# Performance work log

Measured on AMD Instinct MI355X. Metric: run time of the kernel, lower is better.

The kernel has to match this reference:

```python
import jax, jax.numpy as jnp
import numpy as np

MARGIN = 0.2
PAIR_EPS = 1e-6   # torch pairwise_distance eps inside TripletMarginLoss
NORM_EPS = 1e-12  # F.normalize eps


def setup_inputs() -> dict:
    key = jax.random.key(0)
    k1, k2, k3 = jax.random.split(key, 3)
    bs, C, D = 64, 1024, 64
    inputs = jax.random.normal(k1, (bs, C, D), dtype=jnp.float32)
    label = jax.random.randint(k2, (bs, C, 1), 0, 2).astype(jnp.float32)
    prot = jax.random.normal(k3, (C, D), dtype=jnp.float32)
    prot = prot / jnp.linalg.norm(prot, axis=1, keepdims=True)
    return {"inputs": inputs, "label": label, "pos_prot": prot, "only_update": 0}


def reference(inputs, label, pos_prot, only_update):
    bs, C, D = inputs.shape
    # F.normalize(p=2, dim=1) per class slice == normalize over last dim of [bs,C,D]
    nrm = jnp.linalg.norm(inputs, axis=-1, keepdims=True)
    x = inputs / jnp.maximum(nrm, NORM_EPS)                      # [bs,C,D]

    # torch.cdist(x, prot): euclidean distances [bs, C(anchor cls), C(prot)]
    x2 = jnp.sum(x * x, axis=-1)                                 # [bs,C]
    p2 = jnp.sum(pos_prot * pos_prot, axis=-1)                   # [C]
    xp = jnp.einsum('bcd,kd->bck', x, pos_prot)                  # [bs,C,C]
    d2 = x2[:, :, None] + p2[None, None, :] - 2.0 * xp
    prot_dist = jnp.sqrt(jnp.maximum(d2, 0.0))                   # [bs,C,C]

    # hard negative: nearest prototype excluding the anchor's own class
    # (argsort + skip-self loop == masked argmin)
    eye = jnp.eye(C, dtype=bool)[None, :, :]
    neg_cls = jnp.argmin(jnp.where(eye, jnp.inf, prot_dist), axis=-1)  # [bs,C]

    positives = pos_prot[None, :, :]                             # [1,C,D] (broadcast of repeat)
    negatives = pos_prot[neg_cls]                                # [bs,C,D]

    # TripletMarginLoss(margin=0.2, p=2, reduction='none'), eps inside distance
    d_ap = jnp.linalg.norm(x - positives + PAIR_EPS, axis=-1)    # [bs,C]
    d_an = jnp.linalg.norm(x - negatives + PAIR_EPS, axis=-1)    # [bs,C]
    tri = jnp.maximum(d_ap - d_an + MARGIN, 0.0)                 # [bs,C]

    w = label[:, :, 0]                                           # [bs,C]
    loss = jnp.mean(jnp.sum(tri * w, axis=-1) / jnp.sum(w, axis=-1))
    return loss
```

## Files before the change

kernel.cpp:

```cpp
#include <hip/hip_runtime.h>
#include <cfloat>

#define BS 64
#define C  1024
#define D  64
#define CT 128

typedef __attribute__((ext_vector_type(8))) short short8;
typedef __attribute__((ext_vector_type(4))) float f32x4;
typedef unsigned short ushort_t;
typedef unsigned int uint_t;

__device__ __forceinline__ ushort_t f2bf(float f) {
    uint_t u = __float_as_uint(f);
    u += 0x7fffu + ((u >> 16) & 1u);
    return (ushort_t)(u >> 16);
}

__global__ void prep_prot(const float* __restrict__ prot, ushort_t* __restrict__ ph)
{
    const int k = blockIdx.x * 128 + threadIdx.x;
    const float4* row = (const float4*)(prot + (size_t)k * D);
    const int jt = k >> 4;
    #pragma unroll
    for (int dg = 0; dg < 8; dg++) {
        float4 a = row[dg * 2];
        float4 b = row[dg * 2 + 1];
        float x[8] = {a.x, a.y, a.z, a.w, b.x, b.y, b.z, b.w};
        short8 hv;
        #pragma unroll
        for (int e = 0; e < 8; e++) hv[e] = (short)f2bf(x[e]);
        const int h  = dg >> 2;
        const int ln = (k & 15) + (dg & 3) * 16;
        ((short8*)ph)[(size_t)jt * 128 + h * 64 + ln] = hv;
    }
}

__global__ __launch_bounds__(512, 4)
void triplet_mfma(const float* __restrict__ inputs,
                  const float* __restrict__ label,
                  const float* __restrict__ prot,
                  const ushort_t* __restrict__ phg,
                  float* __restrict__ part)
{
    __shared__ short8 xh[1024];
    __shared__ float  invn[CT];
    __shared__ uint_t redk[CT][4];
    __shared__ float  snum[512], sden[512];

    const int tid  = threadIdx.x;
    const int lane = tid & 63;
    const int wid  = tid >> 6;
    const int wr   = wid >> 2;
    const int wc   = wid & 3;
    const int b    = blockIdx.x >> 3;
    const int c0   = (blockIdx.x & 7) * CT;

    const short8* BH = (const short8*)phg;

    short8 ta0 = BH[(size_t)(wc * 16 + 0) * 128 + lane];
    short8 ta1 = BH[(size_t)(wc * 16 + 0) * 128 + 64 + lane];
    short8 tb0 = BH[(size_t)(wc * 16 + 1) * 128 + lane];
    short8 tb1 = BH[(size_t)(wc * 16 + 1) * 128 + 64 + lane];

    if (tid < CT) {
        const float4* r = (const float4*)(inputs + (size_t)(b * C + c0 + tid) * D);
        float s = 0.f;
        #pragma unroll
        for (int q = 0; q < 16; q++) {
            float4 v = r[q];
            s = fmaf(v.x, v.x, fmaf(v.y, v.y, fmaf(v.z, v.z, fmaf(v.w, v.w, s))));
        }
        invn[tid] = 1.0f / fmaxf(sqrtf(s), 1e-12f);
    }
    __syncthreads();

    #pragma unroll
    for (int it = 0; it < 2; it++) {
        int task = tid + it * 512;
        int r = task >> 3, dg = task & 7;
        const float* src = inputs + (size_t)(b * C + c0 + r) * D + dg * 8;
        float inv = invn[r];
        float4 a = *(const float4*)src;
        float4 bb = *(const float4*)(src + 4);
        float x[8] = {a.x, a.y, a.z, a.w, bb.x, bb.y, bb.z, bb.w};
        short8 hv;
        #pragma unroll
        for (int e = 0; e < 8; e++) hv[e] = (short)f2bf(x[e] * inv);
        int f  = (r >> 4) * 2 + (dg >> 2);
        int ln = (r & 15) + (dg & 3) * 16;
        xh[f * 64 + ln] = hv;
    }
    __syncthreads();

    short8 ah[4][2];
    #pragma unroll
    for (int i = 0; i < 4; i++) {
        ah[i][0] = xh[((4 * wr + i) * 2 + 0) * 64 + lane];
        ah[i][1] = xh[((4 * wr + i) * 2 + 1) * 64 + lane];
    }

    uint_t bestk[16];
    #pragma unroll
    for (int q = 0; q < 16; q++) bestk[q] = 0u;

    const uint_t MMASK = 0xFFFFFC00u;
    const int rowtile0 = (c0 >> 4) + wr * 4;
    const int rsub = (lane >> 4) * 4;
    const int csub = lane & 15;

    auto process = [&](int jt, short8 b0, short8 b1) {
        const int jg = wc * 16 + jt;
        const uint_t cidx = (uint_t)(1023 - (jg * 16 + csub));
        #pragma unroll
        for (int i = 0; i < 4; i++) {
            f32x4 acc = {2.0f, 2.0f, 2.0f, 2.0f};
            acc = __builtin_amdgcn_mfma_f32_16x16x32_bf16(ah[i][0], b0, acc, 0, 0, 0);
            acc = __builtin_amdgcn_mfma_f32_16x16x32_bf16(ah[i][1], b1, acc, 0, 0, 0);
            const bool dtile = (rowtile0 + i) == jg;
            #pragma unroll
            for (int r = 0; r < 4; r++) {
                uint_t key = (__float_as_uint(acc[r]) & MMASK) | cidx;
                if (dtile && (rsub + r) == csub) key = 0u;
                bestk[i * 4 + r] = bestk[i * 4 + r] > key ? bestk[i * 4 + r] : key;
            }
        }
    };

    for (int jt = 0; jt < 16; jt += 2) {
        const int p0 = (jt + 2 < 16) ? jt + 2 : 15;
        const int p1 = (jt + 3 < 16) ? jt + 3 : 15;
        short8 n0 = BH[(size_t)(wc * 16 + p0) * 128 + lane];
        short8 n1 = BH[(size_t)(wc * 16 + p0) * 128 + 64 + lane];
        process(jt, ta0, ta1);
        short8 m0 = BH[(size_t)(wc * 16 + p1) * 128 + lane];
        short8 m1 = BH[(size_t)(wc * 16 + p1) * 128 + 64 + lane];
        process(jt + 1, tb0, tb1);
        ta0 = n0; ta1 = n1; tb0 = m0; tb1 = m1;
    }

    #pragma unroll
    for (int i = 0; i < 4; i++)
        #pragma unroll
        for (int r = 0; r < 4; r++) {
            uint_t v = bestk[i * 4 + r];
            #pragma unroll
            for (int off = 1; off < 16; off <<= 1) {
                uint_t ov = (uint_t)__shfl_xor((int)v, off);
                v = v > ov ? v : ov;
            }
            if (csub == 0)
                redk[wr * 64 + i * 16 + rsub + r][wc] = v;
        }
    __syncthreads();

    float num = 0.f, den = 0.f;
    if (tid < CT) {
        uint_t k0 = redk[tid][0], k1 = redk[tid][1];
        uint_t k2 = redk[tid][2], k3 = redk[tid][3];
        uint_t kk = k0 > k1 ? k0 : k1;
        uint_t kl = k2 > k3 ? k2 : k3;
        kk = kk > kl ? kk : kl;
        const int bi = 1023 - (int)(kk & 0x3FFu);
        const int cg = c0 + tid;
        const float inv = invn[tid];
        const float4* xr = (const float4*)(inputs + (size_t)(b * C + cg) * D);
        const float4* pp = (const float4*)(prot + (size_t)cg * D);
        const float4* pn = (const float4*)(prot + (size_t)bi * D);
        float sap = 0.f, san = 0.f;
        #pragma unroll
        for (int q = 0; q < 16; q++) {
            float4 xv = xr[q];
            float4 aa = pp[q];
            float4 nn = pn[q];
            float t;
            t = fmaf(xv.x, inv, -aa.x) + 1e-6f;  sap = fmaf(t, t, sap);
            t = fmaf(xv.y, inv, -aa.y) + 1e-6f;  sap = fmaf(t, t, sap);
            t = fmaf(xv.z, inv, -aa.z) + 1e-6f;  sap = fmaf(t, t, sap);
            t = fmaf(xv.w, inv, -aa.w) + 1e-6f;  sap = fmaf(t, t, sap);
            t = fmaf(xv.x, inv, -nn.x) + 1e-6f;  san = fmaf(t, t, san);
            t = fmaf(xv.y, inv, -nn.y) + 1e-6f;  san = fmaf(t, t, san);
            t = fmaf(xv.z, inv, -nn.z) + 1e-6f;  san = fmaf(t, t, san);
            t = fmaf(xv.w, inv, -nn.w) + 1e-6f;  san = fmaf(t, t, san);
        }
        float tri = fmaxf(sqrtf(sap) - sqrtf(san) + 0.2f, 0.0f);
        float w   = label[b * C + cg];
        num = tri * w;
        den = w;
    }

    snum[tid] = num;
    sden[tid] = den;
    __syncthreads();
    for (int s = 256; s > 0; s >>= 1) {
        if (tid < s) { snum[tid] += snum[tid + s]; sden[tid] += sden[tid + s]; }
        __syncthreads();
    }
    if (tid == 0) {
        part[blockIdx.x * 2 + 0] = snum[0];
        part[blockIdx.x * 2 + 1] = sden[0];
    }
}

__global__ void triplet_finish(const float* __restrict__ part, float* __restrict__ out)
{
    int t = threadIdx.x;
    float num = 0.f, den = 0.f;
    #pragma unroll
    for (int h = 0; h < 8; h++) {
        num += part[(t * 8 + h) * 2 + 0];
        den += part[(t * 8 + h) * 2 + 1];
    }
    float v = num / den;
    #pragma unroll
    for (int off = 32; off > 0; off >>= 1) v += __shfl_down(v, off);
    if (t == 0) out[0] = v * (1.0f / (float)BS);
}

extern "C" void kernel_launch(void* const* d_in, const int* in_sizes, int n_in,
                              void* d_out, int out_size, void* d_ws, size_t ws_size,
                              hipStream_t stream)
{
    const float* inputs = (const float*)d_in[0];
    const float* label  = (const float*)d_in[1];
    const float* prot   = (const float*)d_in[2];
    float* out = (float*)d_out;

    ushort_t* phg  = (ushort_t*)d_ws;
    float*    part = (float*)(phg + (size_t)C * D);

    prep_prot<<<dim3(C / 128), dim3(128), 0, stream>>>(prot, phg);
    triplet_mfma<<<dim3(BS * (C / CT)), dim3(512), 0, stream>>>(
        inputs, label, prot, phg, part);
    triplet_finish<<<1, 64, 0, stream>>>(part, out);
}
```

Measured before the change: 32.08 us.

## Drop pre-normalization pass, fuse final reduction via atomics, halve class tile

Feeds unnormalized bf16 inputs to the MFMA argmin, since the per-row scale does not change which prototype is nearest. The accumulator bias is raised to 16 so packed keys stay positive with the larger magnitudes. The separate inverse-norm pass disappears, and the norm is computed in the epilogue, where four threads split each row and combine with shuffles. The shared-memory tree reduction is replaced by wave shuffles. The separate finish kernel is replaced by per-batch atomics plus a last-block-done counter, which prep_prot zeroes. The class tile drops to 64 with 256-thread blocks, doubling the grid; in exchange, the argmin key loses some precision headroom and the counter adds atomic serialization.

```diff
diff --git a/kernel.cpp b/kernel.cpp
--- a/kernel.cpp
+++ b/kernel.cpp
@@ -4,7 +4,7 @@
 #define BS 64
 #define C  1024
 #define D  64
-#define CT 128
+#define CT 64
 
 typedef __attribute__((ext_vector_type(8))) short short8;
 typedef __attribute__((ext_vector_type(4))) float f32x4;
@@ -17,8 +17,13 @@
     return (ushort_t)(u >> 16);
 }
 
-__global__ void prep_prot(const float* __restrict__ prot, ushort_t* __restrict__ ph)
+__global__ void prep_prot(const float* __restrict__ prot, ushort_t* __restrict__ ph,
+                          float* __restrict__ part, int* __restrict__ cnt)
 {
+    if (blockIdx.x == 0) {
+        if (threadIdx.x < 2 * BS) part[threadIdx.x] = 0.f;
+        if (threadIdx.x == 0) *cnt = 0;
+    }
     const int k = blockIdx.x * 128 + threadIdx.x;
     const float4* row = (const float4*)(prot + (size_t)k * D);
     const int jt = k >> 4;
@@ -36,57 +41,43 @@
     }
 }
 
-__global__ __launch_bounds__(512, 4)
+__global__ __launch_bounds__(256, 4)
 void triplet_mfma(const float* __restrict__ inputs,
                   const float* __restrict__ label,
                   const float* __restrict__ prot,
                   const ushort_t* __restrict__ phg,
-                  float* __restrict__ part)
+                  float* __restrict__ part, int* __restrict__ cnt,
+                  float* __restrict__ out)
 {
-    __shared__ short8 xh[1024];
-    __shared__ float  invn[CT];
+    __shared__ short8 xh[512];
     __shared__ uint_t redk[CT][4];
-    __shared__ float  snum[512], sden[512];
+    __shared__ float  wred[8];
+    __shared__ int    isLastS;
 
     const int tid  = threadIdx.x;
     const int lane = tid & 63;
     const int wid  = tid >> 6;
-    const int wr   = wid >> 2;
-    const int wc   = wid & 3;
-    const int b    = blockIdx.x >> 3;
-    const int c0   = (blockIdx.x & 7) * CT;
+    const int b    = blockIdx.x >> 4;
+    const int c0   = (blockIdx.x & 15) * CT;
 
     const short8* BH = (const short8*)phg;
 
-    short8 ta0 = BH[(size_t)(wc * 16 + 0) * 128 + lane];
-    short8 ta1 = BH[(size_t)(wc * 16 + 0) * 128 + 64 + lane];
-    short8 tb0 = BH[(size_t)(wc * 16 + 1) * 128 + lane];
-    short8 tb1 = BH[(size_t)(wc * 16 + 1) * 128 + 64 + lane];
-
-    if (tid < CT) {
-        const float4* r = (const float4*)(inputs + (size_t)(b * C + c0 + tid) * D);
-        float s = 0.f;
-        #pragma unroll
-        for (int q = 0; q < 16; q++) {
-            float4 v = r[q];
-            s = fmaf(v.x, v.x, fmaf(v.y, v.y, fmaf(v.z, v.z, fmaf(v.w, v.w, s))));
-        }
-        invn[tid] = 1.0f / fmaxf(sqrtf(s), 1e-12f);
-    }
-    __syncthreads();
+    short8 ta0 = BH[(size_t)(wid * 16 + 0) * 128 + lane];
+    short8 ta1 = BH[(size_t)(wid * 16 + 0) * 128 + 64 + lane];
+    short8 tb0 = BH[(size_t)(wid * 16 + 1) * 128 + lane];
+    short8 tb1 = BH[(size_t)(wid * 16 + 1) * 128 + 64 + lane];
 
     #pragma unroll
     for (int it = 0; it < 2; it++) {
-        int task = tid + it * 512;
+        int task = tid + it * 256;
         int r = task >> 3, dg = task & 7;
         const float* src = inputs + (size_t)(b * C + c0 + r) * D + dg * 8;
-        float inv = invn[r];
         float4 a = *(const float4*)src;
         float4 bb = *(const float4*)(src + 4);
         float x[8] = {a.x, a.y, a.z, a.w, bb.x, bb.y, bb.z, bb.w};
         short8 hv;
         #pragma unroll
-        for (int e = 0; e < 8; e++) hv[e] = (short)f2bf(x[e] * inv);
+        for (int e = 0; e < 8; e++) hv[e] = (short)f2bf(x[e]);
         int f  = (r >> 4) * 2 + (dg >> 2);
         int ln = (r & 15) + (dg & 3) * 16;
         xh[f * 64 + ln] = hv;
@@ -96,8 +87,8 @@
     short8 ah[4][2];
     #pragma unroll
     for (int i = 0; i < 4; i++) {
-        ah[i][0] = xh[((4 * wr + i) * 2 + 0) * 64 + lane];
-        ah[i][1] = xh[((4 * wr + i) * 2 + 1) * 64 + lane];
+        ah[i][0] = xh[(i * 2 + 0) * 64 + lane];
+        ah[i][1] = xh[(i * 2 + 1) * 64 + lane];
     }
 
     uint_t bestk[16];
@@ -105,16 +96,16 @@
     for (int q = 0; q < 16; q++) bestk[q] = 0u;
 
     const uint_t MMASK = 0xFFFFFC00u;
-    const int rowtile0 = (c0 >> 4) + wr * 4;
+    const int rowtile0 = c0 >> 4;
     const int rsub = (lane >> 4) * 4;
     const int csub = lane & 15;
 
     auto process = [&](int jt, short8 b0, short8 b1) {
-        const int jg = wc * 16 + jt;
+        const int jg = wid * 16 + jt;
         const uint_t cidx = (uint_t)(1023 - (jg * 16 + csub));
         #pragma unroll
         for (int i = 0; i < 4; i++) {
-            f32x4 acc = {2.0f, 2.0f, 2.0f, 2.0f};
+            f32x4 acc = {16.f, 16.f, 16.f, 16.f};
             acc = __builtin_amdgcn_mfma_f32_16x16x32_bf16(ah[i][0], b0, acc, 0, 0, 0);
             acc = __builtin_amdgcn_mfma_f32_16x16x32_bf16(ah[i][1], b1, acc, 0, 0, 0);
             const bool dtile = (rowtile0 + i) == jg;
@@ -130,11 +121,11 @@
     for (int jt = 0; jt < 16; jt += 2) {
         const int p0 = (jt + 2 < 16) ? jt + 2 : 15;
         const int p1 = (jt + 3 < 16) ? jt + 3 : 15;
-        short8 n0 = BH[(size_t)(wc * 16 + p0) * 128 + lane];
-        short8 n1 = BH[(size_t)(wc * 16 + p0) * 128 + 64 + lane];
+        short8 n0 = BH[(size_t)(wid * 16 + p0) * 128 + lane];
+        short8 n1 = BH[(size_t)(wid * 16 + p0) * 128 + 64 + lane];
         process(jt, ta0, ta1);
-        short8 m0 = BH[(size_t)(wc * 16 + p1) * 128 + lane];
-        short8 m1 = BH[(size_t)(wc * 16 + p1) * 128 + 64 + lane];
+        short8 m0 = BH[(size_t)(wid * 16 + p1) * 128 + lane];
+        short8 m1 = BH[(size_t)(wid * 16 + p1) * 128 + 64 + lane];
         process(jt + 1, tb0, tb1);
         ta0 = n0; ta1 = n1; tb0 = m0; tb1 = m1;
     }
@@ -149,72 +140,86 @@
                 uint_t ov = (uint_t)__shfl_xor((int)v, off);
                 v = v > ov ? v : ov;
             }
-            if (csub == 0)
-                redk[wr * 64 + i * 16 + rsub + r][wc] = v;
+            if (csub == 0) redk[i * 16 + rsub + r][wid] = v;
         }
     __syncthreads();
 
     float num = 0.f, den = 0.f;
-    if (tid < CT) {
-        uint_t k0 = redk[tid][0], k1 = redk[tid][1];
-        uint_t k2 = redk[tid][2], k3 = redk[tid][3];
-        uint_t kk = k0 > k1 ? k0 : k1;
-        uint_t kl = k2 > k3 ? k2 : k3;
-        kk = kk > kl ? kk : kl;
+    {
+        const int row = tid >> 2, p4 = tid & 3;
+        uint_t kk = redk[row][p4];
+        {
+            uint_t o1 = (uint_t)__shfl_xor((int)kk, 1); kk = kk > o1 ? kk : o1;
+            uint_t o2 = (uint_t)__shfl_xor((int)kk, 2); kk = kk > o2 ? kk : o2;
+        }
         const int bi = 1023 - (int)(kk & 0x3FFu);
-        const int cg = c0 + tid;
-        const float inv = invn[tid];
-        const float4* xr = (const float4*)(inputs + (size_t)(b * C + cg) * D);
-        const float4* pp = (const float4*)(prot + (size_t)cg * D);
-        const float4* pn = (const float4*)(prot + (size_t)bi * D);
+        const int cg = c0 + row;
+
+        const float4* xr = (const float4*)(inputs + (size_t)(b * C + cg) * D) + p4 * 4;
+        float4 xv[4];
+        float x2 = 0.f;
+        #pragma unroll
+        for (int q = 0; q < 4; q++) {
+            xv[q] = xr[q];
+            x2 = fmaf(xv[q].x, xv[q].x, fmaf(xv[q].y, xv[q].y,
+                 fmaf(xv[q].z, xv[q].z, fmaf(xv[q].w, xv[q].w, x2))));
+        }
+        x2 += __shfl_xor(x2, 1);
+        x2 += __shfl_xor(x2, 2);
+        const float inv = 1.0f / fmaxf(sqrtf(x2), 1e-12f);
+
+        const float4* pp = (const float4*)(prot + (size_t)cg * D) + p4 * 4;
+        const float4* pn = (const float4*)(prot + (size_t)bi * D) + p4 * 4;
         float sap = 0.f, san = 0.f;
         #pragma unroll
-        for (int q = 0; q < 16; q++) {
-            float4 xv = xr[q];
+        for (int q = 0; q < 4; q++) {
             float4 aa = pp[q];
             float4 nn = pn[q];
             float t;
-            t = fmaf(xv.x, inv, -aa.x) + 1e-6f;  sap = fmaf(t, t, sap);
-            t = fmaf(xv.y, inv, -aa.y) + 1e-6f;  sap = fmaf(t, t, sap);
-            t = fmaf(xv.z, inv, -aa.z) + 1e-6f;  sap = fmaf(t, t, sap);
-            t = fmaf(xv.w, inv, -aa.w) + 1e-6f;  sap = fmaf(t, t, sap);
-            t = fmaf(xv.x, inv, -nn.x) + 1e-6f;  san = fmaf(t, t, san);
-            t = fmaf(xv.y, inv, -nn.y) + 1e-6f;  san = fmaf(t, t, san);
-            t = fmaf(xv.z, inv, -nn.z) + 1e-6f;  san = fmaf(t, t, san);
-            t = fmaf(xv.w, inv, -nn.w) + 1e-6f;  san = fmaf(t, t, san);
-        }
-        float tri = fmaxf(sqrtf(sap) - sqrtf(san) + 0.2f, 0.0f);
-        float w   = label[b * C + cg];
-        num = tri * w;
-        den = w;
-    }
-
-    snum[tid] = num;
-    sden[tid] = den;
-    __syncthreads();
-    for (int s = 256; s > 0; s >>= 1) {
-        if (tid < s) { snum[tid] += snum[tid + s]; sden[tid] += sden[tid + s]; }
-        __syncthreads();
-    }
+            t = fmaf(xv[q].x, inv, -aa.x) + 1e-6f;  sap = fmaf(t, t, sap);
+            t = fmaf(xv[q].y, inv, -aa.y) + 1e-6f;  sap = fmaf(t, t, sap);
+            t = fmaf(xv[q].z, inv, -aa.z) + 1e-6f;  sap = fmaf(t, t, sap);
+            t = fmaf(xv[q].w, inv, -aa.w) + 1e-6f;  sap = fmaf(t, t, sap);
+            t = fmaf(xv[q].x, inv, -nn.x) + 1e-6f;  san = fmaf(t, t, san);
+            t = fmaf(xv[q].y, inv, -nn.y) + 1e-6f;  san = fmaf(t, t, san);
+            t = fmaf(xv[q].z, inv, -nn.z) + 1e-6f;  san = fmaf(t, t, san);
+            t = fmaf(xv[q].w, inv, -nn.w) + 1e-6f;  san = fmaf(t, t, san);
+        }
+        sap += __shfl_xor(sap, 1);  sap += __shfl_xor(sap, 2);
+        san += __shfl_xor(san, 1);  san += __shfl_xor(san, 2);
+        if (p4 == 0) {
+            float tri = fmaxf(sqrtf(sap) - sqrtf(san) + 0.2f, 0.0f);
+            float w   = label[b * C + cg];
+            num = tri * w;
+            den = w;
+        }
+    }
+
+    #pragma unroll
+    for (int off = 1; off < 64; off <<= 1) {
+        num += __shfl_xor(num, off);
+        den += __shfl_xor(den, off);
+    }
+    if (lane == 0) { wred[wid * 2] = num; wred[wid * 2 + 1] = den; }
+    __syncthreads();
+
     if (tid == 0) {
-        part[blockIdx.x * 2 + 0] = snum[0];
-        part[blockIdx.x * 2 + 1] = sden[0];
-    }
-}
-
-__global__ void triplet_finish(const float* __restrict__ part, float* __restrict__ out)
-{
-    int t = threadIdx.x;
-    float num = 0.f, den = 0.f;
-    #pragma unroll
-    for (int h = 0; h < 8; h++) {
-        num += part[(t * 8 + h) * 2 + 0];
-        den += part[(t * 8 + h) * 2 + 1];
-    }
-    float v = num / den;
-    #pragma unroll
-    for (int off = 32; off > 0; off >>= 1) v += __shfl_down(v, off);
-    if (t == 0) out[0] = v * (1.0f / (float)BS);
+        atomicAdd(&part[b * 2 + 0], wred[0] + wred[2] + wred[4] + wred[6]);
+        atomicAdd(&part[b * 2 + 1], wred[1] + wred[3] + wred[5] + wred[7]);
+        __threadfence();
+        int old = __hip_atomic_fetch_add(cnt, 1, __ATOMIC_ACQ_REL, __HIP_MEMORY_SCOPE_AGENT);
+        isLastS = (old == (int)gridDim.x - 1) ? 1 : 0;
+    }
+    __syncthreads();
+
+    if (isLastS && tid < 64) {
+        float n = __hip_atomic_load(&part[tid * 2 + 0], __ATOMIC_RELAXED, __HIP_MEMORY_SCOPE_AGENT);
+        float d = __hip_atomic_load(&part[tid * 2 + 1], __ATOMIC_RELAXED, __HIP_MEMORY_SCOPE_AGENT);
+        float v = n / d;
+        #pragma unroll
+        for (int off = 32; off > 0; off >>= 1) v += __shfl_down(v, off);
+        if (tid == 0) out[0] = v * (1.0f / (float)BS);
+    }
 }
 
 extern "C" void kernel_launch(void* const* d_in, const int* in_sizes, int n_in,
@@ -228,9 +233,9 @@
 
     ushort_t* phg  = (ushort_t*)d_ws;
     float*    part = (float*)(phg + (size_t)C * D);
-
-    prep_prot<<<dim3(C / 128), dim3(128), 0, stream>>>(prot, phg);
-    triplet_mfma<<<dim3(BS * (C / CT)), dim3(512), 0, stream>>>(
-        inputs, label, prot, phg, part);
-    triplet_finish<<<1, 64, 0, stream>>>(part, out);
-}
+    int*      cnt  = (int*)(part + 2 * BS);
+
+    prep_prot<<<dim3(C / 128), dim3(128), 0, stream>>>(prot, phg, part, cnt);
+    triplet_mfma<<<dim3(BS * (C / CT)), dim3(256), 0, stream>>>(
+        inputs, label, prot, phg, part, cnt, out);
+}
```

Result: slower. 56.15 us (+75.0%).
